# Optimization experiments

Hardware: AMD Instinct MI355X
Metric: run time of the kernel (lower is better)

Reference implementation:

```python
import jax, jax.numpy as jnp
import numpy as np

NUM_CAPSULE = 16
DIM_CAPSULE = 32
ROUTINGS = 3
EPS = 1e-7  # K.epsilon()


def _squash(x):
    # NOTE: this repo's squash is x / sqrt(sum(x^2) + eps), i.e. pure normalization
    s = jnp.sum(jnp.square(x), axis=-1, keepdims=True)
    return x / jnp.sqrt(s + EPS)


def setup_inputs() -> dict:
    key = jax.random.key(0)
    k1, k2 = jax.random.split(key)
    B, S, D_in = 256, 512, 256
    u_vecs = jax.random.normal(k1, (B, S, D_in), dtype=jnp.float32)
    # shared conv1d kernel, kernel width 1: (1, input_dim, num_capsule*dim_capsule)
    W = jax.random.normal(k2, (1, D_in, NUM_CAPSULE * DIM_CAPSULE), dtype=jnp.float32) * 0.05
    return {"u_vecs": u_vecs, "W": W}


def reference(u_vecs, W):
    B, S, _ = u_vecs.shape
    # K.conv1d with kernel size 1 == pointwise projection
    u_hat = jnp.einsum('bsi,io->bso', u_vecs, W[0])
    # (B, S, nc*dc) -> (B, nc, S, dc)
    u_hat = u_hat.reshape(B, S, NUM_CAPSULE, DIM_CAPSULE).transpose(0, 2, 1, 3)
    b = jnp.zeros((B, NUM_CAPSULE, S), dtype=u_hat.dtype)
    outputs = None
    for i in range(ROUTINGS):
        # softmax over the num_capsule axis (permute->softmax(last)->permute back)
        c = jax.nn.softmax(b, axis=1)  # (B, nc, S)
        outputs = _squash(jnp.einsum('bni,bnid->bnd', c, u_hat))  # (B, nc, dc)
        if i < ROUTINGS - 1:
            b = jnp.einsum('bnd,bnid->bni', outputs, u_hat)
    return outputs
```

## Files before the change

### kernel.cpp

```cpp
#include <hip/hip_runtime.h>


#define DIN   256
#define OC    512
#define SROWS 512

typedef __attribute__((ext_vector_type(8))) __bf16 bf16x8;
typedef __attribute__((ext_vector_type(4))) float f32x4;
typedef __attribute__((ext_vector_type(4))) unsigned short u16x4;

__device__ __forceinline__ unsigned short f2bf(float f) {
  unsigned u = __float_as_uint(f);
  u += 0x7FFFu + ((u >> 16) & 1u);
  return (unsigned short)(u >> 16);
}

#define SWZ(r) ((((r) ^ ((r) >> 3)) & 7) << 3)

__global__ __launch_bounds__(256) void k_cvt(
    const float* __restrict__ Uall, float* __restrict__ cpart,
    unsigned short* __restrict__ Ub)
{
  __shared__ float sA[4][256];
  const int t = blockIdx.x, b = blockIdx.y;
  const int tid = threadIdx.x;
  const int c4 = tid & 63, rq = tid >> 6;
  const float4* g4 = (const float4*)(Uall + (size_t)b * (SROWS * DIN));
  unsigned short* ub = Ub + (size_t)b * (SROWS * DIN);
  const int R0 = t * 128;
  float4 a = {0.f, 0.f, 0.f, 0.f};
  #pragma unroll 8
  for (int k = 0; k < 32; ++k) {
    const int row = R0 + rq + 4 * k;
    float4 v = g4[row * 64 + c4];
    u16x4 h;
    h[0] = f2bf(v.x); h[1] = f2bf(v.y); h[2] = f2bf(v.z); h[3] = f2bf(v.w);
    *(u16x4*)&ub[(size_t)row * 256 + 4 * c4] = h;
    a.x += v.x; a.y += v.y; a.z += v.z; a.w += v.w;
  }
  *(float4*)&sA[rq][4 * c4] = a;
  __syncthreads();
  if (tid < 64) {
    float4 s = {0.f, 0.f, 0.f, 0.f};
    #pragma unroll
    for (int q = 0; q < 4; ++q) {
      float4 v = *(float4*)&sA[q][4 * tid];
      s.x += v.x; s.y += v.y; s.z += v.z; s.w += v.w;
    }
    *(float4*)&cpart[(size_t)(b * 4 + t) * 256 + 4 * tid] = s;
  }
}

__global__ __launch_bounds__(512) void k_route(
    const float* __restrict__ W, const float* __restrict__ src,
    unsigned short* __restrict__ wt, float* __restrict__ outF,
    int mode, int final_)
{
  __shared__ float sV[16 * 256];
  __shared__ float sP[2][512];
  __shared__ float sOut[512];
  const int b = blockIdx.x;
  const int tid = threadIdx.x;

  if (mode == 0) {
    if (tid < 256) {
      float v = 0.f;
      #pragma unroll
      for (int t = 0; t < 4; ++t) v += src[(size_t)(b * 4 + t) * 256 + tid];
      #pragma unroll
      for (int n = 0; n < 16; ++n) sV[n * 256 + tid] = v;
    }
  } else {
    #pragma unroll
    for (int qq = 0; qq < 2; ++qq) {
      const int q = 2 * tid + qq;
      f32x4 s = {0.f, 0.f, 0.f, 0.f};
      #pragma unroll
      for (int t = 0; t < 4; ++t)
        s += *(const f32x4*)&src[(size_t)(b * 4 + t) * 4096 + 4 * q];
      *(f32x4*)&sV[4 * q] = s;
    }
  }
  __syncthreads();

  {
    const int pair = tid & 255, half = tid >> 8;
    const int c0 = pair * 2, n = c0 >> 5;
    float p0 = 0.f, p1 = 0.f;
    const int i0 = half * 128;
    #pragma unroll 8
    for (int i = i0; i < i0 + 128; ++i) {
      const float2 wv = *(const float2*)&W[(size_t)i * OC + c0];
      const float x = sV[n * 256 + i];
      p0 = fmaf(wv.x, x, p0);
      p1 = fmaf(wv.y, x, p1);
    }
    sP[half][c0] = p0; sP[half][c0 + 1] = p1;
  }
  __syncthreads();

  {
    const float p = sP[0][tid] + sP[1][tid];
    float sq = p * p;
    #pragma unroll
    for (int off = 1; off < 32; off <<= 1) sq += __shfl_xor(sq, off);
    const float o = p * rsqrtf(sq + 1e-7f);
    if (final_) { outF[(size_t)b * 512 + tid] = o; return; }
    sOut[tid] = o;
  }
  __syncthreads();

  {
    const int f4i = tid & 127, rr = tid >> 7;
    const int n = f4i >> 3;
    const float4 ov = *(const float4*)&sOut[4 * f4i];
    #pragma unroll 4
    for (int it = 0; it < 64; ++it) {
      const int i = it * 4 + rr;
      const float4 wv = *(const float4*)&W[(size_t)i * OC + 4 * f4i];
      float p = wv.x * ov.x + wv.y * ov.y + wv.z * ov.z + wv.w * ov.w;
      p += __shfl_xor(p, 1);
      p += __shfl_xor(p, 2);
      p += __shfl_xor(p, 4);
      if ((tid & 7) == 0)
        wt[(size_t)b * 4096 + n * 256 + i] = f2bf(p);
    }
  }
}

__global__ __launch_bounds__(512, 4) void k_pass(
    const unsigned short* __restrict__ Ub, const unsigned short* __restrict__ wt,
    float* __restrict__ vpart)
{
  extern __shared__ char smem[];
  unsigned short* sU  = (unsigned short*)smem;
  unsigned short* sWt = (unsigned short*)(smem + 65536);
  unsigned short* sCT = (unsigned short*)(smem + 73728);

  const int t = blockIdx.x, b = blockIdx.y;
  const int tid = threadIdx.x;
  const int w = tid >> 6, l = tid & 63;
  const int nr = l & 15, g = l >> 4;
  const unsigned short* ub = Ub + (size_t)b * (SROWS * DIN);
  const int R0 = t * 128;

  {
    const int n = tid >> 5, i0 = (tid & 31) * 8;
    const uint4 wv = *(const uint4*)&wt[(size_t)b * 4096 + n * 256 + i0];
    *(uint4*)&sWt[(n * 256 + i0) ^ SWZ(n)] = wv;
  }
  {
    const int col8 = (tid & 31) * 8;
    const int r0 = tid >> 5;
    #pragma unroll
    for (int k = 0; k < 8; ++k) {
      const int row = r0 + 16 * k;
      const uint4 v = *(const uint4*)&ub[(size_t)(R0 + row) * 256 + col8];
      *(uint4*)&sU[(row * 256 + col8) ^ SWZ(row)] = v;
    }
  }
  __syncthreads();

  {
    f32x4 y = {0.f, 0.f, 0.f, 0.f};
    const int arow = 16 * w + nr;
    #pragma unroll
    for (int ks = 0; ks < 8; ++ks) {
      bf16x8 a  = *(const bf16x8*)&sU[(arow * 256 + ks * 32 + g * 8) ^ SWZ(arow)];
      bf16x8 bw = *(const bf16x8*)&sWt[(nr * 256 + ks * 32 + g * 8) ^ SWZ(nr)];
      y = __builtin_amdgcn_mfma_f32_16x16x32_bf16(a, bw, y, 0, 0, 0);
    }
    float e0 = __expf(y[0]), e1 = __expf(y[1]), e2 = __expf(y[2]), e3 = __expf(y[3]);
    float s0 = e0, s1 = e1, s2 = e2, s3 = e3;
    #pragma unroll
    for (int off = 1; off < 16; off <<= 1) {
      s0 += __shfl_xor(s0, off); s1 += __shfl_xor(s1, off);
      s2 += __shfl_xor(s2, off); s3 += __shfl_xor(s3, off);
    }
    u16x4 cw;
    cw[0] = f2bf(e0 / s0); cw[1] = f2bf(e1 / s1);
    cw[2] = f2bf(e2 / s2); cw[3] = f2bf(e3 / s3);
    *(u16x4*)&sCT[(nr * 128 + 16 * w + 4 * g) ^ SWZ(nr)] = cw;
  }
  __syncthreads();

  {
    const int icol0 = 32 * w + nr, icol1 = icol0 + 16;
    f32x4 v0 = {0.f, 0.f, 0.f, 0.f}, v1 = {0.f, 0.f, 0.f, 0.f};
    #pragma unroll
    for (int ks = 0; ks < 4; ++ks) {
      bf16x8 a = *(const bf16x8*)&sCT[(nr * 128 + ks * 32 + g * 8) ^ SWZ(nr)];
      bf16x8 b0, b1;
      #pragma unroll
      for (int j = 0; j < 8; ++j) {
        const int s = ks * 32 + g * 8 + j;
        b0[j] = __builtin_bit_cast(__bf16, sU[(s * 256 + icol0) ^ SWZ(s)]);
        b1[j] = __builtin_bit_cast(__bf16, sU[(s * 256 + icol1) ^ SWZ(s)]);
      }
      v0 = __builtin_amdgcn_mfma_f32_16x16x32_bf16(a, b0, v0, 0, 0, 0);
      v1 = __builtin_amdgcn_mfma_f32_16x16x32_bf16(a, b1, v1, 0, 0, 0);
    }
    float* vp = vpart + (size_t)(b * 4 + t) * 4096;
    #pragma unroll
    for (int r = 0; r < 4; ++r) {
      const int n = 4 * g + r;
      vp[n * 256 + icol0] = v0[r];
      vp[n * 256 + icol1] = v1[r];
    }
  }
}

__global__ __launch_bounds__(1024) void caps_fused(
    const float* __restrict__ Uall, const float* __restrict__ Wg,
    float* __restrict__ outp)
{
  __shared__ __align__(16) unsigned short sU16[64 * 256];
  __shared__ __align__(16) unsigned short sWt16[16 * 256];
  __shared__ __align__(16) unsigned short sCT16[16 * 64];
  __shared__ __align__(16) float sV[16 * 256];
  __shared__ __align__(16) float sOut[512];
  float* sSS = (float*)sCT16;

  const int tid = threadIdx.x;
  const int w = tid >> 6, l = tid & 63;
  const int b = blockIdx.x;
  const float* U = Uall + (size_t)b * (SROWS * DIN);
  const float4* g4 = (const float4*)U;

  {
    float4 a = make_float4(0.f, 0.f, 0.f, 0.f);
    const int base = (w * 32) * 64 + l;
    #pragma unroll 8
    for (int r = 0; r < 32; ++r) {
      float4 v = g4[base + r * 64];
      a.x += v.x; a.y += v.y; a.z += v.z; a.w += v.w;
    }
    *(float4*)&sV[w * 256 + 4 * l] = a;
  }
  __syncthreads();
  if (tid < 256) {
    float s = 0.f;
    #pragma unroll
    for (int q = 0; q < 16; ++q) s += sV[q * 256 + tid];
    sSS[tid] = s * (1.0f / 16.0f);
  }
  __syncthreads();

  auto outCompute = [&](int mode) {
    if (tid < 512) {
      const int c = tid, n = c >> 5;
      float p0 = 0.f, p1 = 0.f, p2 = 0.f, p3 = 0.f;
      #pragma unroll 4
      for (int i = 0; i < 256; i += 4) {
        float x0 = mode ? sV[n * 256 + i + 0] : sSS[i + 0];
        float x1 = mode ? sV[n * 256 + i + 1] : sSS[i + 1];
        float x2 = mode ? sV[n * 256 + i + 2] : sSS[i + 2];
        float x3 = mode ? sV[n * 256 + i + 3] : sSS[i + 3];
        p0 = fmaf(Wg[(i + 0) * OC + c], x0, p0);
        p1 = fmaf(Wg[(i + 1) * OC + c], x1, p1);
        p2 = fmaf(Wg[(i + 2) * OC + c], x2, p2);
        p3 = fmaf(Wg[(i + 3) * OC + c], x3, p3);
      }
      float p = (p0 + p1) + (p2 + p3);
      float sq = p * p;
      #pragma unroll
      for (int off = 1; off < 32; off <<= 1) sq += __shfl_xor(sq, off);
      sOut[c] = p * rsqrtf(sq + 1e-7f);
    }
    __syncthreads();
  };

  auto wtCompute = [&]() {
    const int f4 = tid & 127;
    const int rr = tid >> 7;
    const float4 ov = *(const float4*)&sOut[4 * f4];
    #pragma unroll 4
    for (int it = 0; it < 32; ++it) {
      const int i = it * 8 + rr;
      const float4 wv = *(const float4*)&Wg[i * OC + 4 * f4];
      float p = wv.x * ov.x + wv.y * ov.y + wv.z * ov.z + wv.w * ov.w;
      p += __shfl_xor(p, 1);
      p += __shfl_xor(p, 2);
      p += __shfl_xor(p, 4);
      if ((f4 & 7) == 0) {
        const int n = f4 >> 3;
        sWt16[(n * 256 + i) ^ ((n & 7) << 3)] = f2bf(p);
      }
    }
    __syncthreads();
  };

  auto stage = [&](const float4* pre) {
    #pragma unroll
    for (int k = 0; k < 4; ++k) {
      const int s = w + 16 * k;
      u16x4 h;
      h[0] = f2bf(pre[k].x); h[1] = f2bf(pre[k].y);
      h[2] = f2bf(pre[k].z); h[3] = f2bf(pre[k].w);
      *(u16x4*)&sU16[(s * 256 + 4 * l) ^ ((s & 7) << 3)] = h;
    }
  };

  auto pass = [&]() {
    f32x4 vacc = {0.f, 0.f, 0.f, 0.f};
    const int nr = l & 15;
    const int grp = l >> 4;
    {
      float4 pre[4];
      #pragma unroll
      for (int k = 0; k < 4; ++k) pre[k] = g4[(w + 16 * k) * 64 + l];
      stage(pre);
    }
    __syncthreads();
    for (int chunk = 0; chunk < 8; ++chunk) {
      float4 nxt[4];
      if (chunk < 7) {
        #pragma unroll
        for (int k = 0; k < 4; ++k)
          nxt[k] = g4[((chunk + 1) * 64 + w + 16 * k) * 64 + l];
      }
      if (w < 4) {
        f32x4 y = {0.f, 0.f, 0.f, 0.f};
        const int arow = 16 * w + nr;
        #pragma unroll
        for (int ks = 0; ks < 8; ++ks) {
          bf16x8 a = *(const bf16x8*)&sU16[(arow * 256 + ks * 32 + grp * 8) ^ ((arow & 7) << 3)];
          bf16x8 bw = *(const bf16x8*)&sWt16[(nr * 256 + ks * 32 + grp * 8) ^ ((nr & 7) << 3)];
          y = __builtin_amdgcn_mfma_f32_16x16x32_bf16(a, bw, y, 0, 0, 0);
        }
        float e0 = __expf(y[0]), e1 = __expf(y[1]), e2 = __expf(y[2]), e3 = __expf(y[3]);
        float s0 = e0, s1 = e1, s2 = e2, s3 = e3;
        #pragma unroll
        for (int off = 1; off < 16; off <<= 1) {
          s0 += __shfl_xor(s0, off); s1 += __shfl_xor(s1, off);
          s2 += __shfl_xor(s2, off); s3 += __shfl_xor(s3, off);
        }
        u16x4 cw;
        cw[0] = f2bf(e0 / s0); cw[1] = f2bf(e1 / s1);
        cw[2] = f2bf(e2 / s2); cw[3] = f2bf(e3 / s3);
        *(u16x4*)&sCT16[(nr * 64 + 16 * w + 4 * grp) ^ ((nr & 7) << 3)] = cw;
      }
      __syncthreads();
      {
        const int icol = 16 * w + nr;
        #pragma unroll
        for (int ks = 0; ks < 2; ++ks) {
          bf16x8 a = *(const bf16x8*)&sCT16[(nr * 64 + ks * 32 + grp * 8) ^ ((nr & 7) << 3)];
          bf16x8 bb;
          const int s0b = ks * 32 + grp * 8;
          #pragma unroll
          for (int j = 0; j < 8; ++j) {
            unsigned short v = sU16[((s0b + j) * 256 + icol) ^ (j << 3)];
            bb[j] = __builtin_bit_cast(__bf16, v);
          }
          vacc = __builtin_amdgcn_mfma_f32_16x16x32_bf16(a, bb, vacc, 0, 0, 0);
        }
      }
      __syncthreads();
      if (chunk < 7) stage(nxt);
      __syncthreads();
    }
    #pragma unroll
    for (int r = 0; r < 4; ++r) sV[(grp * 4 + r) * 256 + 16 * w + nr] = vacc[r];
    __syncthreads();
  };

  outCompute(0);
  wtCompute();
  pass();
  outCompute(1);
  wtCompute();
  pass();
  outCompute(1);

  if (tid < 512) outp[(size_t)b * 512 + tid] = sOut[tid];
}

extern "C" void kernel_launch(void* const* d_in, const int* in_sizes, int n_in,
                              void* d_out, int out_size, void* d_ws, size_t ws_size,
                              hipStream_t stream) {
  const float* U = (const float*)d_in[0];
  const float* W = (const float*)d_in[1];
  float* out = (float*)d_out;

  const size_t WT_OFF = 0;
  const size_t CP_OFF = 2u * 1024 * 1024;
  const size_t VP_OFF = 3u * 1024 * 1024;
  const size_t UB_OFF = 19u * 1024 * 1024;
  const size_t NEED   = UB_OFF + 64u * 1024 * 1024;

  if (ws_size < NEED) {
    caps_fused<<<dim3(256), dim3(1024), 0, stream>>>(U, W, out);
    return;
  }
  unsigned short* wt = (unsigned short*)((char*)d_ws + WT_OFF);
  float* cpart = (float*)((char*)d_ws + CP_OFF);
  float* vpart = (float*)((char*)d_ws + VP_OFF);
  unsigned short* Ub = (unsigned short*)((char*)d_ws + UB_OFF);

  hipFuncSetAttribute(reinterpret_cast<const void*>(k_pass),
                      hipFuncAttributeMaxDynamicSharedMemorySize, 77824);

  k_cvt<<<dim3(4, 256), 256, 0, stream>>>(U, cpart, Ub);
  k_route<<<256, 512, 0, stream>>>(W, cpart, wt, out, 0, 0);
  k_pass<<<dim3(4, 256), 512, 77824, stream>>>(Ub, wt, vpart);
  k_route<<<256, 512, 0, stream>>>(W, vpart, wt, out, 1, 0);
  k_pass<<<dim3(4, 256), 512, 77824, stream>>>(Ub, wt, vpart);
  k_route<<<256, 512, 0, stream>>>(W, vpart, wt, out, 1, 1);
}
```

Before: 302.6 us.

## Fuse routing passes into per-batch kernels with double-buffered staging

Merges the conversion kernel with the first routing step, and merges each pass kernel with the following routing step into one per-batch block. Each block walks all 512 rows in four chunks and double-buffers the bf16 tiles in shared memory, so partial sums no longer go through global memory and the launch count drops from six to three. In exchange the grid shrinks from 1024 blocks to 256 blocks with one block per CU and 140KB of LDS. That may reduce latency hiding and occupancy.

```diff
diff --git a/kernel.cpp b/kernel.cpp
--- a/kernel.cpp
+++ b/kernel.cpp
@@ -17,96 +17,57 @@
 
 #define SWZ(r) ((((r) ^ ((r) >> 3)) & 7) << 3)
 
-__global__ __launch_bounds__(256) void k_cvt(
-    const float* __restrict__ Uall, float* __restrict__ cpart,
-    unsigned short* __restrict__ Ub)
+__global__ __launch_bounds__(512) void k_cvt_route(
+    const float* __restrict__ Uall, const float* __restrict__ W,
+    unsigned short* __restrict__ Ub, unsigned short* __restrict__ wt)
 {
-  __shared__ float sA[4][256];
-  const int t = blockIdx.x, b = blockIdx.y;
+  __shared__ float sA[8][256];
+  __shared__ float sCS[256];
+  __shared__ float sOut[512];
+  const int b = blockIdx.x;
   const int tid = threadIdx.x;
-  const int c4 = tid & 63, rq = tid >> 6;
+  const int c4 = tid & 63, r0 = tid >> 6;
   const float4* g4 = (const float4*)(Uall + (size_t)b * (SROWS * DIN));
   unsigned short* ub = Ub + (size_t)b * (SROWS * DIN);
-  const int R0 = t * 128;
+
   float4 a = {0.f, 0.f, 0.f, 0.f};
   #pragma unroll 8
-  for (int k = 0; k < 32; ++k) {
-    const int row = R0 + rq + 4 * k;
+  for (int k = 0; k < 64; ++k) {
+    const int row = r0 + 8 * k;
     float4 v = g4[row * 64 + c4];
     u16x4 h;
     h[0] = f2bf(v.x); h[1] = f2bf(v.y); h[2] = f2bf(v.z); h[3] = f2bf(v.w);
     *(u16x4*)&ub[(size_t)row * 256 + 4 * c4] = h;
     a.x += v.x; a.y += v.y; a.z += v.z; a.w += v.w;
   }
-  *(float4*)&sA[rq][4 * c4] = a;
+  *(float4*)&sA[r0][4 * c4] = a;
   __syncthreads();
   if (tid < 64) {
     float4 s = {0.f, 0.f, 0.f, 0.f};
     #pragma unroll
-    for (int q = 0; q < 4; ++q) {
+    for (int q = 0; q < 8; ++q) {
       float4 v = *(float4*)&sA[q][4 * tid];
       s.x += v.x; s.y += v.y; s.z += v.z; s.w += v.w;
     }
-    *(float4*)&cpart[(size_t)(b * 4 + t) * 256 + 4 * tid] = s;
-  }
-}
-
-__global__ __launch_bounds__(512) void k_route(
-    const float* __restrict__ W, const float* __restrict__ src,
-    unsigned short* __restrict__ wt, float* __restrict__ outF,
-    int mode, int final_)
-{
-  __shared__ float sV[16 * 256];
-  __shared__ float sP[2][512];
-  __shared__ float sOut[512];
-  const int b = blockIdx.x;
-  const int tid = threadIdx.x;
-
-  if (mode == 0) {
-    if (tid < 256) {
-      float v = 0.f;
-      #pragma unroll
-      for (int t = 0; t < 4; ++t) v += src[(size_t)(b * 4 + t) * 256 + tid];
-      #pragma unroll
-      for (int n = 0; n < 16; ++n) sV[n * 256 + tid] = v;
-    }
-  } else {
-    #pragma unroll
-    for (int qq = 0; qq < 2; ++qq) {
-      const int q = 2 * tid + qq;
-      f32x4 s = {0.f, 0.f, 0.f, 0.f};
-      #pragma unroll
-      for (int t = 0; t < 4; ++t)
-        s += *(const f32x4*)&src[(size_t)(b * 4 + t) * 4096 + 4 * q];
-      *(f32x4*)&sV[4 * q] = s;
-    }
-  }
-  __syncthreads();
-
-  {
-    const int pair = tid & 255, half = tid >> 8;
-    const int c0 = pair * 2, n = c0 >> 5;
-    float p0 = 0.f, p1 = 0.f;
-    const int i0 = half * 128;
-    #pragma unroll 8
-    for (int i = i0; i < i0 + 128; ++i) {
-      const float2 wv = *(const float2*)&W[(size_t)i * OC + c0];
-      const float x = sV[n * 256 + i];
-      p0 = fmaf(wv.x, x, p0);
-      p1 = fmaf(wv.y, x, p1);
-    }
-    sP[half][c0] = p0; sP[half][c0 + 1] = p1;
-  }
-  __syncthreads();
-
-  {
-    const float p = sP[0][tid] + sP[1][tid];
+    *(float4*)&sCS[4 * tid] = s;
+  }
+  __syncthreads();
+
+  {
+    const int c = tid;
+    float p0 = 0.f, p1 = 0.f, p2 = 0.f, p3 = 0.f;
+    #pragma unroll 4
+    for (int i = 0; i < 256; i += 4) {
+      p0 = fmaf(W[(size_t)(i + 0) * OC + c], sCS[i + 0], p0);
+      p1 = fmaf(W[(size_t)(i + 1) * OC + c], sCS[i + 1], p1);
+      p2 = fmaf(W[(size_t)(i + 2) * OC + c], sCS[i + 2], p2);
+      p3 = fmaf(W[(size_t)(i + 3) * OC + c], sCS[i + 3], p3);
+    }
+    float p = (p0 + p1) + (p2 + p3);
     float sq = p * p;
     #pragma unroll
     for (int off = 1; off < 32; off <<= 1) sq += __shfl_xor(sq, off);
-    const float o = p * rsqrtf(sq + 1e-7f);
-    if (final_) { outF[(size_t)b * 512 + tid] = o; return; }
-    sOut[tid] = o;
+    sOut[c] = p * rsqrtf(sq + 1e-7f);
   }
   __syncthreads();
 
@@ -128,84 +89,142 @@
   }
 }
 
-__global__ __launch_bounds__(512, 4) void k_pass(
-    const unsigned short* __restrict__ Ub, const unsigned short* __restrict__ wt,
-    float* __restrict__ vpart)
+__global__ __launch_bounds__(512, 1) void k_main(
+    const unsigned short* __restrict__ Ub, const float* __restrict__ W,
+    unsigned short* __restrict__ wt, float* __restrict__ outF, int final_)
 {
   extern __shared__ char smem[];
-  unsigned short* sU  = (unsigned short*)smem;
-  unsigned short* sWt = (unsigned short*)(smem + 65536);
-  unsigned short* sCT = (unsigned short*)(smem + 73728);
-
-  const int t = blockIdx.x, b = blockIdx.y;
+  unsigned short* sU0 = (unsigned short*)smem;
+  unsigned short* sU1 = (unsigned short*)(smem + 65536);
+  unsigned short* sWt = (unsigned short*)(smem + 131072);
+  unsigned short* sCT = (unsigned short*)(smem + 139264);
+  float* sV   = (float*)smem;
+  float* sP   = (float*)(smem + 16384);
+  float* sOut = (float*)(smem + 20480);
+
+  const int b = blockIdx.x;
   const int tid = threadIdx.x;
   const int w = tid >> 6, l = tid & 63;
   const int nr = l & 15, g = l >> 4;
   const unsigned short* ub = Ub + (size_t)b * (SROWS * DIN);
-  const int R0 = t * 128;
 
   {
     const int n = tid >> 5, i0 = (tid & 31) * 8;
     const uint4 wv = *(const uint4*)&wt[(size_t)b * 4096 + n * 256 + i0];
     *(uint4*)&sWt[(n * 256 + i0) ^ SWZ(n)] = wv;
   }
-  {
-    const int col8 = (tid & 31) * 8;
-    const int r0 = tid >> 5;
+
+  const int col8 = (tid & 31) * 8;
+  const int sr0 = tid >> 5;
+  auto stageTo = [&](unsigned short* dst, int R0) {
     #pragma unroll
     for (int k = 0; k < 8; ++k) {
-      const int row = r0 + 16 * k;
+      const int row = sr0 + 16 * k;
       const uint4 v = *(const uint4*)&ub[(size_t)(R0 + row) * 256 + col8];
-      *(uint4*)&sU[(row * 256 + col8) ^ SWZ(row)] = v;
-    }
-  }
-  __syncthreads();
-
-  {
-    f32x4 y = {0.f, 0.f, 0.f, 0.f};
-    const int arow = 16 * w + nr;
-    #pragma unroll
-    for (int ks = 0; ks < 8; ++ks) {
-      bf16x8 a  = *(const bf16x8*)&sU[(arow * 256 + ks * 32 + g * 8) ^ SWZ(arow)];
-      bf16x8 bw = *(const bf16x8*)&sWt[(nr * 256 + ks * 32 + g * 8) ^ SWZ(nr)];
-      y = __builtin_amdgcn_mfma_f32_16x16x32_bf16(a, bw, y, 0, 0, 0);
-    }
-    float e0 = __expf(y[0]), e1 = __expf(y[1]), e2 = __expf(y[2]), e3 = __expf(y[3]);
-    float s0 = e0, s1 = e1, s2 = e2, s3 = e3;
-    #pragma unroll
-    for (int off = 1; off < 16; off <<= 1) {
-      s0 += __shfl_xor(s0, off); s1 += __shfl_xor(s1, off);
-      s2 += __shfl_xor(s2, off); s3 += __shfl_xor(s3, off);
-    }
-    u16x4 cw;
-    cw[0] = f2bf(e0 / s0); cw[1] = f2bf(e1 / s1);
-    cw[2] = f2bf(e2 / s2); cw[3] = f2bf(e3 / s3);
-    *(u16x4*)&sCT[(nr * 128 + 16 * w + 4 * g) ^ SWZ(nr)] = cw;
-  }
-  __syncthreads();
-
-  {
-    const int icol0 = 32 * w + nr, icol1 = icol0 + 16;
-    f32x4 v0 = {0.f, 0.f, 0.f, 0.f}, v1 = {0.f, 0.f, 0.f, 0.f};
-    #pragma unroll
-    for (int ks = 0; ks < 4; ++ks) {
-      bf16x8 a = *(const bf16x8*)&sCT[(nr * 128 + ks * 32 + g * 8) ^ SWZ(nr)];
-      bf16x8 b0, b1;
+      *(uint4*)&dst[(row * 256 + col8) ^ SWZ(row)] = v;
+    }
+  };
+  stageTo(sU0, 0);
+  __syncthreads();
+
+  f32x4 v0acc = {0.f, 0.f, 0.f, 0.f}, v1acc = {0.f, 0.f, 0.f, 0.f};
+  const int icol0 = 32 * w + nr, icol1 = icol0 + 16;
+
+  for (int c = 0; c < 4; ++c) {
+    unsigned short* cur = (c & 1) ? sU1 : sU0;
+    unsigned short* nxt = (c & 1) ? sU0 : sU1;
+    if (c < 3) stageTo(nxt, (c + 1) * 128);
+
+    {
+      f32x4 y = {0.f, 0.f, 0.f, 0.f};
+      const int arow = 16 * w + nr;
       #pragma unroll
-      for (int j = 0; j < 8; ++j) {
-        const int s = ks * 32 + g * 8 + j;
-        b0[j] = __builtin_bit_cast(__bf16, sU[(s * 256 + icol0) ^ SWZ(s)]);
-        b1[j] = __builtin_bit_cast(__bf16, sU[(s * 256 + icol1) ^ SWZ(s)]);
-      }
-      v0 = __builtin_amdgcn_mfma_f32_16x16x32_bf16(a, b0, v0, 0, 0, 0);
-      v1 = __builtin_amdgcn_mfma_f32_16x16x32_bf16(a, b1, v1, 0, 0, 0);
-    }
-    float* vp = vpart + (size_t)(b * 4 + t) * 4096;
-    #pragma unroll
-    for (int r = 0; r < 4; ++r) {
-      const int n = 4 * g + r;
-      vp[n * 256 + icol0] = v0[r];
-      vp[n * 256 + icol1] = v1[r];
+      for (int ks = 0; ks < 8; ++ks) {
+        bf16x8 a  = *(const bf16x8*)&cur[(arow * 256 + ks * 32 + g * 8) ^ SWZ(arow)];
+        bf16x8 bw = *(const bf16x8*)&sWt[(nr * 256 + ks * 32 + g * 8) ^ SWZ(nr)];
+        y = __builtin_amdgcn_mfma_f32_16x16x32_bf16(a, bw, y, 0, 0, 0);
+      }
+      float e0 = __expf(y[0]), e1 = __expf(y[1]), e2 = __expf(y[2]), e3 = __expf(y[3]);
+      float s0 = e0, s1 = e1, s2 = e2, s3 = e3;
+      #pragma unroll
+      for (int off = 1; off < 16; off <<= 1) {
+        s0 += __shfl_xor(s0, off); s1 += __shfl_xor(s1, off);
+        s2 += __shfl_xor(s2, off); s3 += __shfl_xor(s3, off);
+      }
+      u16x4 cw;
+      cw[0] = f2bf(e0 / s0); cw[1] = f2bf(e1 / s1);
+      cw[2] = f2bf(e2 / s2); cw[3] = f2bf(e3 / s3);
+      *(u16x4*)&sCT[(nr * 128 + 16 * w + 4 * g) ^ SWZ(nr)] = cw;
+    }
+    __syncthreads();
+
+    {
+      #pragma unroll
+      for (int ks = 0; ks < 4; ++ks) {
+        bf16x8 a = *(const bf16x8*)&sCT[(nr * 128 + ks * 32 + g * 8) ^ SWZ(nr)];
+        bf16x8 b0, b1;
+        #pragma unroll
+        for (int j = 0; j < 8; ++j) {
+          const int s = ks * 32 + g * 8 + j;
+          b0[j] = __builtin_bit_cast(__bf16, cur[(s * 256 + icol0) ^ SWZ(s)]);
+          b1[j] = __builtin_bit_cast(__bf16, cur[(s * 256 + icol1) ^ SWZ(s)]);
+        }
+        v0acc = __builtin_amdgcn_mfma_f32_16x16x32_bf16(a, b0, v0acc, 0, 0, 0);
+        v1acc = __builtin_amdgcn_mfma_f32_16x16x32_bf16(a, b1, v1acc, 0, 0, 0);
+      }
+    }
+    __syncthreads();
+  }
+
+  #pragma unroll
+  for (int r = 0; r < 4; ++r) {
+    const int n = 4 * g + r;
+    sV[n * 256 + icol0] = v0acc[r];
+    sV[n * 256 + icol1] = v1acc[r];
+  }
+  __syncthreads();
+
+  {
+    const int pair = tid & 255, half = tid >> 8;
+    const int c0 = pair * 2, n = c0 >> 5;
+    float p0 = 0.f, p1 = 0.f;
+    const int i0h = half * 128;
+    #pragma unroll 8
+    for (int i = i0h; i < i0h + 128; ++i) {
+      const float2 wv = *(const float2*)&W[(size_t)i * OC + c0];
+      const float x = sV[n * 256 + i];
+      p0 = fmaf(wv.x, x, p0);
+      p1 = fmaf(wv.y, x, p1);
+    }
+    sP[half * 512 + c0] = p0; sP[half * 512 + c0 + 1] = p1;
+  }
+  __syncthreads();
+
+  {
+    const float p = sP[tid] + sP[512 + tid];
+    float sq = p * p;
+    #pragma unroll
+    for (int off = 1; off < 32; off <<= 1) sq += __shfl_xor(sq, off);
+    const float o = p * rsqrtf(sq + 1e-7f);
+    if (final_) { outF[(size_t)b * 512 + tid] = o; return; }
+    sOut[tid] = o;
+  }
+  __syncthreads();
+
+  {
+    const int f4i = tid & 127, rr = tid >> 7;
+    const int n = f4i >> 3;
+    const float4 ov = *(const float4*)&sOut[4 * f4i];
+    #pragma unroll 4
+    for (int it = 0; it < 64; ++it) {
+      const int i = it * 4 + rr;
+      const float4 wv = *(const float4*)&W[(size_t)i * OC + 4 * f4i];
+      float p = wv.x * ov.x + wv.y * ov.y + wv.z * ov.z + wv.w * ov.w;
+      p += __shfl_xor(p, 1);
+      p += __shfl_xor(p, 2);
+      p += __shfl_xor(p, 4);
+      if ((tid & 7) == 0)
+        wt[(size_t)b * 4096 + n * 256 + i] = f2bf(p);
     }
   }
 }
@@ -384,9 +403,7 @@
   float* out = (float*)d_out;
 
   const size_t WT_OFF = 0;
-  const size_t CP_OFF = 2u * 1024 * 1024;
-  const size_t VP_OFF = 3u * 1024 * 1024;
-  const size_t UB_OFF = 19u * 1024 * 1024;
+  const size_t UB_OFF = 2u * 1024 * 1024;
   const size_t NEED   = UB_OFF + 64u * 1024 * 1024;
 
   if (ws_size < NEED) {
@@ -394,17 +411,12 @@
     return;
   }
   unsigned short* wt = (unsigned short*)((char*)d_ws + WT_OFF);
-  float* cpart = (float*)((char*)d_ws + CP_OFF);
-  float* vpart = (float*)((char*)d_ws + VP_OFF);
   unsigned short* Ub = (unsigned short*)((char*)d_ws + UB_OFF);
 
-  hipFuncSetAttribute(reinterpret_cast<const void*>(k_pass),
-                      hipFuncAttributeMaxDynamicSharedMemorySize, 77824);
-
-  k_cvt<<<dim3(4, 256), 256, 0, stream>>>(U, cpart, Ub);
-  k_route<<<256, 512, 0, stream>>>(W, cpart, wt, out, 0, 0);
-  k_pass<<<dim3(4, 256), 512, 77824, stream>>>(Ub, wt, vpart);
-  k_route<<<256, 512, 0, stream>>>(W, vpart, wt, out, 1, 0);
-  k_pass<<<dim3(4, 256), 512, 77824, stream>>>(Ub, wt, vpart);
-  k_route<<<256, 512, 0, stream>>>(W, vpart, wt, out, 1, 1);
+  hipFuncSetAttribute(reinterpret_cast<const void*>(k_main),
+                      hipFuncAttributeMaxDynamicSharedMemorySize, 143360);
+
+  k_cvt_route<<<256, 512, 0, stream>>>(U, W, Ub, wt);
+  k_main<<<256, 512, 143360, stream>>>(Ub, W, wt, out, 0);
+  k_main<<<256, 512, 143360, stream>>>(Ub, W, wt, out, 1);
 }
```

New measurement: 296.9 us. Within noise of the previous version (-1.9%).
